# Kernel optimization log

Hardware: AMD Instinct MI355X
Metric: run time of the kernel (lower is better)

## Reference

```python
import jax, jax.numpy as jnp
import numpy as np

B, S, HID = 2, 2048, 2048
H, HKV, D = 16, 8, 128
RQ, RK, RV = 6, 2, 2
WINDOW = 1024
SOFTCAP = 50.0
SCALING = D ** -0.5
NEG_INF = -2.3819763e38  # gemma mask fill value (fp32 safe)


def _rope(x, cos, sin):
    # Gemma rotary: split last dim into two halves treated as (real, imag).
    d2 = x.shape[-1] // 2
    x1, x2 = x[..., :d2], x[..., d2:]
    return jnp.concatenate([x1 * cos - x2 * sin, x1 * sin + x2 * cos], axis=-1)


def setup_inputs() -> dict:
    key = jax.random.key(0)
    ks = jax.random.split(key, 8)
    hidden_states = jax.random.normal(ks[0], (B, S, HID), jnp.float32)
    w = 0.02
    W_A_q = jax.random.normal(ks[1], (HID, H * RQ), jnp.float32) * w
    W_B_q = jax.random.normal(ks[2], (HID, H * RQ * D), jnp.float32) * w
    W_A_k = jax.random.normal(ks[3], (HID, HKV * RK), jnp.float32) * w
    W_B_k = jax.random.normal(ks[4], (HID, RK * D), jnp.float32) * w
    W_A_v = jax.random.normal(ks[5], (HID, HKV * RV), jnp.float32) * w
    W_B_v = jax.random.normal(ks[6], (HID, RV * D), jnp.float32) * w
    W_o = jax.random.normal(ks[7], (H * D, HID), jnp.float32) * w
    # rotary tables (theta=10000)
    pos = jnp.arange(S, dtype=jnp.float32)
    inv = 1.0 / (10000.0 ** (jnp.arange(0, D, 2, dtype=jnp.float32) / D))
    ang = pos[:, None] * inv[None, :]  # [S, D/2]
    freqs_cos, freqs_sin = jnp.cos(ang), jnp.sin(ang)
    # causal + sliding-window additive mask [B,1,S,S]
    i = jnp.arange(S)[:, None]
    j = jnp.arange(S)[None, :]
    allowed = (j <= i) & (i - j < WINDOW)
    mask = jnp.where(allowed, 0.0, NEG_INF).astype(jnp.float32)
    mask = jnp.broadcast_to(mask[None, None], (B, 1, S, S))
    kv_write_indices = jnp.arange(S, dtype=jnp.int32)  # prefill: identity write
    return {
        'hidden_states': hidden_states, 'W_A_q': W_A_q, 'W_B_q': W_B_q,
        'W_A_k': W_A_k, 'W_B_k': W_B_k, 'W_A_v': W_A_v, 'W_B_v': W_B_v,
        'W_o': W_o, 'freqs_cos': freqs_cos, 'freqs_sin': freqs_sin,
        'mask': mask, 'kv_write_indices': kv_write_indices,
    }


def reference(hidden_states, W_A_q, W_B_q, W_A_k, W_B_k, W_A_v, W_B_v, W_o,
              freqs_cos, freqs_sin, mask, kv_write_indices):
    # Prefill: kv_write_indices == arange(S); factorized cache == current factors.
    b, s, _ = hidden_states.shape
    Aq = (hidden_states @ W_A_q).reshape(b, s, H, RQ)       # [b,s,H,Rq]
    Bq = (hidden_states @ W_B_q).reshape(b, s, H, RQ, D)    # [b,s,H,Rq,d]
    Ak = (hidden_states @ W_A_k).reshape(b, s, HKV, RK)
    Bk = (hidden_states @ W_B_k).reshape(b, s, RK, D)
    Av = (hidden_states @ W_A_v).reshape(b, s, HKV, RV)
    Bv = (hidden_states @ W_B_v).reshape(b, s, RV, D)
    # RoPE on the B factors (as in the original: applied to B_q rows and B_k rows)
    Bq = _rope(Bq, freqs_cos[:, None, None, :], freqs_sin[:, None, None, :])
    Bk = _rope(Bk, freqs_cos[:, None, :], freqs_sin[:, None, :])
    # Contract rank factors. Identical math to the per-head
    # einsum('bqrd,bksd->bqkrs') + einsum('bqr,bks,bqkrs->bqk') since the
    # bilinear form factorizes: sum_{r,s} Aq_r Ak_s <Bq_r, Bk_s> = <q, k>.
    q = jnp.einsum('bshr,bshrd->bshd', Aq, Bq)               # [b,s,H,d]
    k = jnp.einsum('bsgr,bsrd->bsgd', Ak, Bk)                # [b,s,Hkv,d]
    v = jnp.einsum('bsgr,bsrd->bsgd', Av, Bv)
    rep = H // HKV
    k = jnp.repeat(k, rep, axis=2)                            # GQA expand
    v = jnp.repeat(v, rep, axis=2)
    scores = jnp.einsum('bqhd,bkhd->bhqk', q, k) * SCALING
    scores = jnp.tanh(scores / SOFTCAP) * SOFTCAP             # logit softcap
    scores = scores + mask                                    # local sliding mask
    probs = jax.nn.softmax(scores, axis=-1)
    out = jnp.einsum('bhqk,bkhd->bqhd', probs, v).reshape(b, s, H * D)
    return out @ W_o
```

## Files before the change

kernel.cpp:

```cpp
#include <hip/hip_runtime.h>
#include <hip/hip_bf16.h>

#define S_LEN 2048
#define HID 2048
#define NB 2
#define NH 16
#define NKV 8
#define DH 128
#define RQ 6
#define KG 2048
#define SCALING 0.08838834764831845f

typedef __attribute__((ext_vector_type(8))) short s16x8;
typedef __attribute__((ext_vector_type(4))) float f32x4;

__device__ __forceinline__ float bf2f(ushort u) {
    union { unsigned int i; float f; } v; v.i = ((unsigned int)u) << 16; return v.f;
}
__device__ __forceinline__ ushort f2bf(float f) {
    __hip_bfloat16 h = __float2bfloat16(f);
    return *reinterpret_cast<ushort*>(&h);
}
__device__ __forceinline__ void g2lds16(const void* g, void* l) {
    __builtin_amdgcn_global_load_lds((const __attribute__((address_space(1))) void*)g,
                                     (__attribute__((address_space(3))) void*)l, 16, 0, 0);
}

__global__ void k_prep(const float* __restrict__ hs, const float* __restrict__ WAq,
                       const float* __restrict__ WAk, const float* __restrict__ WAv,
                       const float* __restrict__ WBk, const float* __restrict__ WBv,
                       const float* __restrict__ WBq, const float* __restrict__ Wo,
                       ushort* __restrict__ Xb, ushort* __restrict__ WtS,
                       ushort* __restrict__ WtBq, ushort* __restrict__ WtWo) {
    __shared__ ushort tile[64][68];
    int idx = blockIdx.x;
    int t = threadIdx.x;
    if (idx < 2048) {
#pragma unroll
        for (int j = 0; j < 4; ++j) {
            int i = idx * 1024 + t + j * 256;
            float4 v = ((const float4*)hs)[i];
            ushort4 o;
            o.x = f2bf(v.x); o.y = f2bf(v.y); o.z = f2bf(v.z); o.w = f2bf(v.w);
            ((ushort4*)Xb)[i] = o;
        }
        return;
    }
    idx -= 2048;
    const float* in; ushort* out; int Nin, rowOff;
    if (idx < 64)        { in = WAq; out = WtS;  Nin = 96;    rowOff = 0; }
    else if (idx < 96)   { idx -= 64;   in = WAk; out = WtS;  Nin = 16;    rowOff = 96; }
    else if (idx < 128)  { idx -= 96;   in = WAv; out = WtS;  Nin = 16;    rowOff = 112; }
    else if (idx < 256)  { idx -= 128;  in = WBk; out = WtS;  Nin = 256;   rowOff = 128; }
    else if (idx < 384)  { idx -= 256;  in = WBv; out = WtS;  Nin = 256;   rowOff = 384; }
    else if (idx < 6528) { idx -= 384;  in = WBq; out = WtBq; Nin = 12288; rowOff = 0; }
    else                 { idx -= 6528; in = Wo;  out = WtWo; Nin = 2048;  rowOff = 0; }
    int k0 = (idx & 31) * 64, n0 = (idx >> 5) * 64;
#pragma unroll
    for (int i = 0; i < 4; ++i) {
        int f = t + i * 256;
        int r = f >> 4;
        int c = (f & 15) * 4;
        int nn = n0 + c;
        float4 v = make_float4(0.f, 0.f, 0.f, 0.f);
        if (nn < Nin) v = *(const float4*)&in[(size_t)(k0 + r) * Nin + nn];
        ushort4 u;
        u.x = f2bf(v.x); u.y = f2bf(v.y); u.z = f2bf(v.z); u.w = f2bf(v.w);
        *(ushort4*)&tile[r][c] = u;
    }
    __syncthreads();
#pragma unroll
    for (int i = 0; i < 4; ++i) {
        int f = t + i * 256;
        int nr = f >> 4;
        int kc = (f & 15) * 4;
        int nn = n0 + nr;
        if (nn < Nin) {
            ushort4 u;
            u.x = tile[kc][nr]; u.y = tile[kc + 1][nr];
            u.z = tile[kc + 2][nr]; u.w = tile[kc + 3][nr];
            *(ushort4*)&out[(size_t)(rowOff + nn) * KG + k0 + kc] = u;
        }
    }
}

__device__ __forceinline__ void stc(float* p, float v) { *p = v; }
__device__ __forceinline__ void stc(ushort* p, float v) { *p = f2bf(v); }

template<typename OutT>
__global__ __launch_bounds__(256, 2) void k_gemm(const ushort* __restrict__ A,
                                                 const ushort* __restrict__ Bt,
                                                 OutT* __restrict__ C, int ldc) {
    __shared__ ushort lA[128 * 64];
    __shared__ ushort lB[128 * 64];
    const int tid = threadIdx.x;
    const int l = tid & 63, w = tid >> 6;
    const int gx = gridDim.x;
    int flat = blockIdx.y * gx + blockIdx.x;
    const int nwg = gx * gridDim.y;
    if ((nwg & 7) == 0) {
        int qq = nwg >> 3;
        flat = (flat & 7) * qq + (flat >> 3);
    }
    const int m0 = (flat % gx) * 128, n0 = (flat / gx) * 128;
    const int wm = w >> 1, wn = w & 1;
    f32x4 acc[4][4] = {};
    const int swz = 16 * ((tid & 7) ^ ((tid >> 3) & 7));
    const int rowbase = tid >> 3;

    for (int k0 = 0; k0 < KG; k0 += 64) {
#pragma unroll
        for (int i = 0; i < 4; ++i) {
            int row = rowbase + i * 32;
            const char* srcA = (const char*)A + (((size_t)(m0 + row) * KG + k0) * 2) + swz;
            g2lds16(srcA, (char*)lA + tid * 16 + i * 4096);
            const char* srcB = (const char*)Bt + (((size_t)(n0 + row) * KG + k0) * 2) + swz;
            g2lds16(srcB, (char*)lB + tid * 16 + i * 4096);
        }
        __syncthreads();
#pragma unroll
        for (int kk = 0; kk < 2; ++kk) {
            s16x8 af[4], bfr[4];
            const int kb = kk * 64 + (l >> 4) * 16;
#pragma unroll
            for (int mf = 0; mf < 4; ++mf) {
                int row = wm * 64 + mf * 16 + (l & 15);
                af[mf] = *(const s16x8*)((const char*)lA + row * 128 + (kb ^ ((row & 7) << 4)));
            }
#pragma unroll
            for (int nf = 0; nf < 4; ++nf) {
                int row = wn * 64 + nf * 16 + (l & 15);
                bfr[nf] = *(const s16x8*)((const char*)lB + row * 128 + (kb ^ ((row & 7) << 4)));
            }
#pragma unroll
            for (int mf = 0; mf < 4; ++mf)
#pragma unroll
                for (int nf = 0; nf < 4; ++nf)
                    acc[mf][nf] = __builtin_amdgcn_mfma_f32_16x16x32_bf16(af[mf], bfr[nf], acc[mf][nf], 0, 0, 0);
        }
        __syncthreads();
    }
#pragma unroll
    for (int mf = 0; mf < 4; ++mf)
#pragma unroll
        for (int r = 0; r < 4; ++r) {
            int row = m0 + wm * 64 + mf * 16 + (l >> 4) * 4 + r;
#pragma unroll
            for (int nf = 0; nf < 4; ++nf) {
                int col = n0 + wn * 64 + nf * 16 + (l & 15);
                stc(C + (size_t)row * ldc + col, acc[mf][nf][r]);
            }
        }
}

__global__ __launch_bounds__(512, 2) void k_gemm8(const ushort* __restrict__ A,
                                                  const ushort* __restrict__ Bt,
                                                  ushort* __restrict__ C, int ldc) {
    __shared__ char sB[131072];
    const int tid = threadIdx.x;
    const int l = tid & 63, wid = tid >> 6;
    const int wr = wid >> 2, wc = wid & 3;

    int flat = blockIdx.x;
    const int nwg = gridDim.x;
    if ((nwg & 7) == 0) {
        int qq = nwg >> 3;
        flat = (flat & 7) * qq + (flat >> 3);
    }
    const int m0 = (flat & 15) * 256;
    const int n0 = (flat >> 4) * 256;

    const int rb = tid >> 3;
    const int swz = 16 * ((tid & 7) ^ (rb & 7));
    const char* pAh[2][2];
    const char* pBh[2][2];
#pragma unroll
    for (int h = 0; h < 2; ++h)
#pragma unroll
        for (int j = 0; j < 2; ++j) {
            pAh[h][j] = (const char*)A + (size_t)(m0 + j * 128 + h * 64 + rb) * (KG * 2) + swz;
            pBh[h][j] = (const char*)Bt + (size_t)(n0 + (j * 2 + (tid >> 8)) * 64 + h * 32 + (rb & 31)) * (KG * 2) + swz;
        }

    f32x4 acc[8][4] = {};
    s16x8 af[4][2], bf[4][2];

    const int arow = (l & 15) * 128;
    const int kxor0 = (0 * 64 + (l >> 4) * 16) ^ ((l & 7) << 4);
    const int kxor1 = (1 * 64 + (l >> 4) * 16) ^ ((l & 7) << 4);

#define STG_A(T, D, H)                                                                     \
    do {                                                                                   \
        g2lds16(pAh[H][0] + (size_t)(T) * 128, sB + (D) * 65536 + (H) * 16384 + tid * 16); \
        g2lds16(pAh[H][1] + (size_t)(T) * 128, sB + (D) * 65536 + (H) * 16384 + 8192 + tid * 16); \
    } while (0)
#define STG_B(T, D, H)                                                                     \
    do {                                                                                   \
        g2lds16(pBh[H][0] + (size_t)(T) * 128, sB + (D) * 65536 + 32768 + (H) * 16384 + tid * 16); \
        g2lds16(pBh[H][1] + (size_t)(T) * 128, sB + (D) * 65536 + 32768 + (H) * 16384 + 8192 + tid * 16); \
    } while (0)
#define RD_A(D, MH)                                                                        \
    do {                                                                                   \
        const char* ab = sB + (D) * 65536 + (MH) * 16384 + wr * 8192;                      \
        _Pragma("unroll") for (int mi = 0; mi < 4; ++mi) {                                 \
            af[mi][0] = *(const s16x8*)(ab + mi * 2048 + arow + kxor0);                    \
            af[mi][1] = *(const s16x8*)(ab + mi * 2048 + arow + kxor1);                    \
        }                                                                                  \
    } while (0)
#define RD_B(D, BH)                                                                        \
    do {                                                                                   \
        const char* bb = sB + (D) * 65536 + 32768 + (BH) * 16384 + wc * 4096;              \
        _Pragma("unroll") for (int ni = 0; ni < 2; ++ni) {                                 \
            bf[(BH) * 2 + ni][0] = *(const s16x8*)(bb + ni * 2048 + arow + kxor0);         \
            bf[(BH) * 2 + ni][1] = *(const s16x8*)(bb + ni * 2048 + arow + kxor1);         \
        }                                                                                  \
    } while (0)
#define QMFMA(MQ, NQ)                                                                      \
    do {                                                                                   \
        __builtin_amdgcn_s_setprio(1);                                                     \
        _Pragma("unroll") for (int mi = 0; mi < 4; ++mi)                                   \
        _Pragma("unroll") for (int ni = 0; ni < 2; ++ni)                                   \
        _Pragma("unroll") for (int k2 = 0; k2 < 2; ++k2)                                   \
            acc[(MQ) * 4 + mi][(NQ) * 2 + ni] = __builtin_amdgcn_mfma_f32_16x16x32_bf16(   \
                af[mi][k2], bf[(NQ) * 2 + ni][k2], acc[(MQ) * 4 + mi][(NQ) * 2 + ni], 0, 0, 0); \
        __builtin_amdgcn_s_setprio(0);                                                     \
    } while (0)
#define BAR()                                   \
    do {                                        \
        asm volatile("" ::: "memory");          \
        __builtin_amdgcn_s_barrier();           \
        asm volatile("" ::: "memory");          \
    } while (0)
#define VM6() asm volatile("s_waitcnt vmcnt(6)" ::: "memory")
#define VM0() asm volatile("s_waitcnt vmcnt(0)" ::: "memory")

    STG_A(0, 0, 0); STG_A(0, 0, 1); STG_B(0, 0, 0); STG_B(0, 0, 1);
    STG_B(1, 1, 0); STG_B(1, 1, 1); STG_A(1, 1, 0);
    VM6();
    BAR();

    for (int i = 0; i < 16; ++i) {
        const bool last = (i == 15);
        const int t1 = 2 * i + 1, t2 = 2 * i + 2, t3 = 2 * i + 3;
        RD_A(0, 0); RD_B(0, 0);
        STG_A(t1, 1, 1);
        BAR(); QMFMA(0, 0); BAR();
        RD_B(0, 1);
        if (!last) STG_A(t2, 0, 0);
        BAR(); QMFMA(0, 1); BAR();
        RD_A(0, 1);
        if (!last) STG_B(t2, 0, 0);
        BAR(); QMFMA(1, 1); BAR();
        if (!last) { STG_B(t2, 0, 1); VM6(); } else { VM0(); }
        BAR(); QMFMA(1, 0); BAR();
        RD_A(1, 0); RD_B(1, 0);
        if (!last) STG_A(t2, 0, 1);
        BAR(); QMFMA(0, 0); BAR();
        RD_B(1, 1);
        if (!last) STG_B(t3, 1, 0);
        BAR(); QMFMA(0, 1); BAR();
        RD_A(1, 1);
        if (!last) STG_B(t3, 1, 1);
        BAR(); QMFMA(1, 1); BAR();
        if (!last) { STG_A(t3, 1, 0); VM6(); }
        BAR(); QMFMA(1, 0); BAR();
    }

#undef STG_A
#undef STG_B
#undef RD_A
#undef RD_B
#undef QMFMA

#pragma unroll
    for (int mf = 0; mf < 8; ++mf)
#pragma unroll
        for (int r = 0; r < 4; ++r) {
            int row = m0 + wr * 128 + mf * 16 + (l >> 4) * 4 + r;
#pragma unroll
            for (int nf = 0; nf < 4; ++nf) {
                int col = n0 + wc * 64 + nf * 16 + (l & 15);
                C[(size_t)row * ldc + col] = f2bf(acc[mf][nf][r]);
            }
        }
#undef BAR
#undef VM6
#undef VM0
}

__global__ __launch_bounds__(512, 2) void k_gemm8h(const ushort* __restrict__ A,
                                                   const ushort* __restrict__ Bt,
                                                   float* __restrict__ C, int ldc) {
    __shared__ char sB[98304];
    const int tid = threadIdx.x;
    const int l = tid & 63, wid = tid >> 6;
    const int wr = wid >> 2, wc = wid & 3;

    int flat = blockIdx.x;
    const int nwg = gridDim.x;
    if ((nwg & 7) == 0) {
        int qq = nwg >> 3;
        flat = (flat & 7) * qq + (flat >> 3);
    }
    const int m0 = (flat & 31) * 128;
    const int n0 = (flat >> 5) * 256;

    const int rb = tid >> 3;
    const int swz = 16 * ((tid & 7) ^ (rb & 7));
    const char* pA_[2];
    const char* pB_[2][2];
#pragma unroll
    for (int h = 0; h < 2; ++h) {
        pA_[h] = (const char*)A + (size_t)(m0 + (tid >> 8) * 64 + h * 32 + (rb & 31)) * (KG * 2) + swz;
#pragma unroll
        for (int j = 0; j < 2; ++j)
            pB_[h][j] = (const char*)Bt + (size_t)(n0 + (j * 2 + (tid >> 8)) * 64 + h * 32 + (rb & 31)) * (KG * 2) + swz;
    }

    f32x4 acc[4][4] = {};
    s16x8 af[2][2], bf[4][2];

    const int arow = (l & 15) * 128;
    const int kxor0 = ((l >> 4) * 16) ^ ((l & 7) << 4);
    const int kxor1 = (64 + (l >> 4) * 16) ^ ((l & 7) << 4);

#define STG_AH(T, D, H)                                                                    \
    g2lds16(pA_[H] + (size_t)(T) * 128, sB + (D) * 49152 + (H) * 8192 + tid * 16)
#define STG_BH(T, D, H)                                                                    \
    do {                                                                                   \
        g2lds16(pB_[H][0] + (size_t)(T) * 128, sB + (D) * 49152 + 16384 + (H) * 16384 + tid * 16); \
        g2lds16(pB_[H][1] + (size_t)(T) * 128, sB + (D) * 49152 + 16384 + (H) * 16384 + 8192 + tid * 16); \
    } while (0)
#define RD_AH(D, MH)                                                                       \
    do {                                                                                   \
        const char* ab = sB + (D) * 49152 + (MH) * 8192 + wr * 4096;                       \
        _Pragma("unroll") for (int mi = 0; mi < 2; ++mi) {                                 \
            af[mi][0] = *(const s16x8*)(ab + mi * 2048 + arow + kxor0);                    \
            af[mi][1] = *(const s16x8*)(ab + mi * 2048 + arow + kxor1);                    \
        }                                                                                  \
    } while (0)
#define RD_BH(D, BH)                                                                       \
    do {                                                                                   \
        const char* bb = sB + (D) * 49152 + 16384 + (BH) * 16384 + wc * 4096;              \
        _Pragma("unroll") for (int ni = 0; ni < 2; ++ni) {                                 \
            bf[(BH) * 2 + ni][0] = *(const s16x8*)(bb + ni * 2048 + arow + kxor0);         \
            bf[(BH) * 2 + ni][1] = *(const s16x8*)(bb + ni * 2048 + arow + kxor1);         \
        }                                                                                  \
    } while (0)
#define QMFMAH(MQ, NQ)                                                                     \
    do {                                                                                   \
        __builtin_amdgcn_s_setprio(1);                                                     \
        _Pragma("unroll") for (int mi = 0; mi < 2; ++mi)                                   \
        _Pragma("unroll") for (int ni = 0; ni < 2; ++ni)                                   \
        _Pragma("unroll") for (int k2 = 0; k2 < 2; ++k2)                                   \
            acc[(MQ) * 2 + mi][(NQ) * 2 + ni] = __builtin_amdgcn_mfma_f32_16x16x32_bf16(   \
                af[mi][k2], bf[(NQ) * 2 + ni][k2], acc[(MQ) * 2 + mi][(NQ) * 2 + ni], 0, 0, 0); \
        __builtin_amdgcn_s_setprio(0);                                                     \
    } while (0)
#define BAR()                                   \
    do {                                        \
        asm volatile("" ::: "memory");          \
        __builtin_amdgcn_s_barrier();           \
        asm volatile("" ::: "memory");          \
    } while (0)
#define VM5() asm volatile("s_waitcnt vmcnt(5)" ::: "memory")
#define VM0() asm volatile("s_waitcnt vmcnt(0)" ::: "memory")

    STG_AH(0, 0, 0); STG_AH(0, 0, 1); STG_BH(0, 0, 0); STG_BH(0, 0, 1);
    STG_BH(1, 1, 0); STG_BH(1, 1, 1); STG_AH(1, 1, 0);
    VM5();
    BAR();

    for (int i = 0; i < 16; ++i) {
        const bool last = (i == 15);
        const int t1 = 2 * i + 1, t2 = 2 * i + 2, t3 = 2 * i + 3;
        RD_AH(0, 0); RD_BH(0, 0);
        STG_AH(t1, 1, 1);
        BAR(); QMFMAH(0, 0); BAR();
        RD_BH(0, 1);
        if (!last) STG_AH(t2, 0, 0);
        BAR(); QMFMAH(0, 1); BAR();
        RD_AH(0, 1);
        if (!last) STG_BH(t2, 0, 0);
        BAR(); QMFMAH(1, 1); BAR();
        if (!last) { STG_BH(t2, 0, 1); VM5(); } else { VM0(); }
        BAR(); QMFMAH(1, 0); BAR();
        RD_AH(1, 0); RD_BH(1, 0);
        if (!last) STG_AH(t2, 0, 1);
        BAR(); QMFMAH(0, 0); BAR();
        RD_BH(1, 1);
        if (!last) STG_BH(t3, 1, 0);
        BAR(); QMFMAH(0, 1); BAR();
        RD_AH(1, 1);
        if (!last) STG_BH(t3, 1, 1);
        BAR(); QMFMAH(1, 1); BAR();
        if (!last) { STG_AH(t3, 1, 0); VM5(); }
        BAR(); QMFMAH(1, 0); BAR();
    }

#undef STG_AH
#undef STG_BH
#undef RD_AH
#undef RD_BH
#undef QMFMAH
#undef BAR
#undef VM5
#undef VM0

#pragma unroll
    for (int a = 0; a < 4; ++a)
#pragma unroll
        for (int r = 0; r < 4; ++r) {
            int row = m0 + wr * 64 + a * 16 + (l >> 4) * 4 + r;
#pragma unroll
            for (int b2 = 0; b2 < 4; ++b2) {
                int col = n0 + wc * 64 + b2 * 16 + (l & 15);
                C[(size_t)row * ldc + col] = acc[a][b2][r];
            }
        }
}

__global__ void k_contract_q(const ushort* __restrict__ bq, const float* __restrict__ small,
                             const float* __restrict__ cosT, const float* __restrict__ sinT,
                             ushort* __restrict__ q, int pitch, int hbase) {
    int srow = blockIdx.x;
    int b = srow >> 11, sl = srow & 2047;
    int t = threadIdx.x;
    int l = t & 63;
    int hloc = blockIdx.y * 4 + (t >> 6);
    int h = hbase + hloc;
    const ushort* bqr = bq + (size_t)srow * pitch + hloc * 768;
    const float* af = small + (size_t)srow * 640 + h * RQ;
    float y0 = 0.f, y1 = 0.f;
#pragma unroll
    for (int r = 0; r < RQ; ++r) {
        float a = af[r];
        ushort2 v = *(const ushort2*)&bqr[r * 128 + 2 * l];
        y0 += a * bf2f(v.x);
        y1 += a * bf2f(v.y);
    }
    float z0 = __shfl_xor(y0, 32);
    float z1 = __shfl_xor(y1, 32);
    int d = (l & 31) * 2;
    float2 cs = *(const float2*)&cosT[sl * 64 + d];
    float2 sn = *(const float2*)&sinT[sl * 64 + d];
    size_t o = ((size_t)(b * NH + h) * S_LEN + sl) * DH;
    ushort2 outv;
    if (l < 32) {
        outv.x = f2bf((y0 * cs.x - z0 * sn.x) * SCALING);
        outv.y = f2bf((y1 * cs.y - z1 * sn.y) * SCALING);
        *(ushort2*)&q[o + d] = outv;
    } else {
        outv.x = f2bf((z0 * sn.x + y0 * cs.x) * SCALING);
        outv.y = f2bf((z1 * sn.y + y1 * cs.y) * SCALING);
        *(ushort2*)&q[o + 64 + d] = outv;
    }
}

__global__ void k_contract_kv(const float* __restrict__ small, const float* __restrict__ cosT,
                              const float* __restrict__ sinT, ushort* __restrict__ kk,
                              ushort* __restrict__ vT) {
    int srow = blockIdx.x;
    int b = srow >> 11, sl = srow & 2047;
    int t = threadIdx.x;
    int d2 = t & 63, g = t >> 6;
    const float* row = small + (size_t)srow * 640;
    float k1 = 0.f, k2 = 0.f, v1 = 0.f, v2 = 0.f;
#pragma unroll
    for (int r = 0; r < 2; ++r) {
        float ak = row[96 + g * 2 + r];
        k1 += ak * row[128 + r * 128 + d2];
        k2 += ak * row[128 + r * 128 + 64 + d2];
        float av = row[112 + g * 2 + r];
        v1 += av * row[384 + r * 128 + d2];
        v2 += av * row[384 + r * 128 + 64 + d2];
    }
    float c = cosT[sl * 64 + d2], s = sinT[sl * 64 + d2];
    float kr1 = k1 * c - k2 * s, kr2 = k1 * s + k2 * c;
    size_t ko = ((size_t)(b * NKV + g) * S_LEN + sl) * DH + d2;
    kk[ko] = f2bf(kr1);
    kk[ko + 64] = f2bf(kr2);
    size_t vo = ((size_t)(b * NKV + g) * DH + d2) * S_LEN + sl;
    vT[vo] = f2bf(v1);
    vT[vo + (size_t)64 * S_LEN] = f2bf(v2);
}

__device__ __forceinline__ float softcap_p(float x) {
    float z = x * 0.02f;
    float z2 = z * z;
    float num = z * fmaf(z2, z2 + 105.f, 945.f);
    float den = fmaf(z2, fmaf(z2, 15.f, 420.f), 945.f);
    return __expf(fmaf(50.f, __fdividef(num, den), -50.f));
}

template<int FUSEQ>
__global__ __launch_bounds__(512, 2) void k_attn(const ushort* __restrict__ qsrc,
                                                 const float* __restrict__ small,
                                                 const float* __restrict__ cosT,
                                                 const float* __restrict__ sinT,
                                                 const ushort* __restrict__ kk,
                                                 const ushort* __restrict__ vT,
                                                 ushort* __restrict__ O) {
    __shared__ char sK[16384];
    __shared__ char sV[16384];
    __shared__ char sP[16384];
    const int f = blockIdx.x;
    const int xcd = f & 7;
    const int j = f >> 3;
    const int bg = xcd * 2 + (j >> 5);
    const int qb = 31 - (j & 31);
    const int b = bg >> 3, g = bg & 7;
    const int tid = threadIdx.x, l = tid & 63, w = tid >> 6;
    const int w4 = w & 3;
    const int h = g * 2 + (w >> 2);
    const int qs = qb * 64;
    const int q0 = qs + w4 * 16;

    s16x8 qf[4];
    if (FUSEQ) {
        const int row = q0 + (l & 15);
        const int srow = b * S_LEN + row;
        const float* af = small + (size_t)srow * 640 + h * RQ;
        const ushort* bqr = qsrc + (size_t)srow * 12288 + h * 768;
        const int k8 = (l >> 4) * 8;
#pragma unroll
        for (int grp = 0; grp < 2; ++grp) {
            const int dbase = grp * 32 + k8;
            float x1[8] = {}, x2[8] = {};
#pragma unroll
            for (int r = 0; r < RQ; ++r) {
                float a = af[r];
                s16x8 v1 = *(const s16x8*)&bqr[r * 128 + dbase];
                s16x8 v2 = *(const s16x8*)&bqr[r * 128 + 64 + dbase];
#pragma unroll
                for (int e = 0; e < 8; ++e) {
                    x1[e] = fmaf(a, bf2f((ushort)v1[e]), x1[e]);
                    x2[e] = fmaf(a, bf2f((ushort)v2[e]), x2[e]);
                }
            }
            const float* cp = &cosT[row * 64 + dbase];
            const float* sp = &sinT[row * 64 + dbase];
            s16x8 lo, hi;
#pragma unroll
            for (int e = 0; e < 8; ++e) {
                float c = cp[e], s = sp[e];
                lo[e] = (short)f2bf((x1[e] * c - x2[e] * s) * SCALING);
                hi[e] = (short)f2bf((x1[e] * s + x2[e] * c) * SCALING);
            }
            qf[grp] = lo;
            qf[grp + 2] = hi;
        }
    } else {
        const ushort* qbase = qsrc + ((size_t)(b * NH + h) * S_LEN) * DH;
        const char* qrow = (const char*)(qbase + (size_t)(q0 + (l & 15)) * DH);
#pragma unroll
        for (int ds = 0; ds < 4; ++ds)
            qf[ds] = *(const s16x8*)(qrow + ds * 64 + (l >> 4) * 16);
    }

    f32x4 acc[8] = {};
    float lrow[4] = {0.f, 0.f, 0.f, 0.f};

    const size_t kgbase = ((size_t)(b * NKV + g) * S_LEN) * DH * 2;
    const size_t vgbase = ((size_t)(b * NKV + g) * DH) * S_LEN * 2;

    const int jt0 = (qs > 1023) ? ((qs - 1023) >> 6) : 0;
    const int ibase = q0 + (l >> 4) * 4;

    for (int jt = jt0; jt <= qb; ++jt) {
#pragma unroll
        for (int i = 0; i < 2; ++i) {
            int row = (tid >> 4) + i * 32;
            int colb = (tid & 15) * 16;
            const char* src = (const char*)kk + kgbase + ((size_t)(jt * 64 + row)) * 256 + (colb ^ ((row & 7) << 4));
            g2lds16(src, sK + tid * 16 + i * 8192);
        }
#pragma unroll
        for (int i = 0; i < 2; ++i) {
            int row = (tid >> 3) + i * 64;
            int colb = (tid & 7) * 16;
            const char* src = (const char*)vT + vgbase + (size_t)row * 4096 + (size_t)jt * 128 + (colb ^ ((row & 7) << 4));
            g2lds16(src, sV + tid * 16 + i * 8192);
        }
        __syncthreads();

        const bool diag = (jt == qb);
        const bool wclip = (jt == jt0) && (qs > 1023);

        f32x4 sc[4] = {};
#pragma unroll
        for (int ct = 0; ct < 4; ++ct) {
            if (diag && ct > w4) continue;
            f32x4 z = {};
            int row = ct * 16 + (l & 15);
#pragma unroll
            for (int ds = 0; ds < 4; ++ds) {
                int kb = ds * 64 + (l >> 4) * 16;
                s16x8 kf = *(const s16x8*)(sK + row * 256 + (kb ^ ((row & 7) << 4)));
                z = __builtin_amdgcn_mfma_f32_16x16x32_bf16(qf[ds], kf, z, 0, 0, 0);
            }
            sc[ct] = z;
        }
        float p[4][4];
        if (!diag && !wclip) {
#pragma unroll
            for (int ct = 0; ct < 4; ++ct)
#pragma unroll
                for (int r = 0; r < 4; ++r) {
                    float pe = softcap_p(sc[ct][r]);
                    p[ct][r] = pe;
                    lrow[r] += pe;
                }
        } else if (diag) {
#pragma unroll
            for (int ct = 0; ct < 4; ++ct) {
                if (ct > w4) {
#pragma unroll
                    for (int r = 0; r < 4; ++r) p[ct][r] = 0.f;
                    continue;
                }
                int j2 = jt * 64 + ct * 16 + (l & 15);
#pragma unroll
                for (int r = 0; r < 4; ++r) {
                    float pe = softcap_p(sc[ct][r]);
                    pe = (j2 <= ibase + r) ? pe : 0.f;
                    p[ct][r] = pe;
                    lrow[r] += pe;
                }
            }
        } else {
#pragma unroll
            for (int ct = 0; ct < 4; ++ct) {
                int j2 = jt * 64 + ct * 16 + (l & 15);
#pragma unroll
                for (int r = 0; r < 4; ++r) {
                    float pe = softcap_p(sc[ct][r]);
                    pe = (j2 > ibase + r - 1024) ? pe : 0.f;
                    p[ct][r] = pe;
                    lrow[r] += pe;
                }
            }
        }
#pragma unroll
        for (int ct = 0; ct < 4; ++ct) {
            int col = ct * 16 + (l & 15);
#pragma unroll
            for (int r = 0; r < 4; ++r) {
                int row = (l >> 4) * 4 + r;
                *(ushort*)(sP + w * 2048 + row * 128 + ((col * 2) ^ ((row & 7) << 4))) = f2bf(p[ct][r]);
            }
        }
#pragma unroll
        for (int s2 = 0; s2 < 2; ++s2) {
            int rowp = l & 15;
            int kb = s2 * 64 + (l >> 4) * 16;
            s16x8 pf = *(const s16x8*)(sP + w * 2048 + rowp * 128 + (kb ^ ((rowp & 7) << 4)));
#pragma unroll
            for (int dt = 0; dt < 8; ++dt) {
                int d = dt * 16 + (l & 15);
                s16x8 vf = *(const s16x8*)(sV + d * 128 + (kb ^ ((d & 7) << 4)));
                acc[dt] = __builtin_amdgcn_mfma_f32_16x16x32_bf16(pf, vf, acc[dt], 0, 0, 0);
            }
        }
        __syncthreads();
    }
#pragma unroll
    for (int r = 0; r < 4; ++r) {
        float rs = lrow[r];
        rs += __shfl_xor(rs, 1); rs += __shfl_xor(rs, 2);
        rs += __shfl_xor(rs, 4); rs += __shfl_xor(rs, 8);
        lrow[r] = rs;
    }
#pragma unroll
    for (int r = 0; r < 4; ++r) {
        int row = qs + w4 * 16 + (l >> 4) * 4 + r;
        float inv = 1.f / lrow[r];
#pragma unroll
        for (int dt = 0; dt < 8; ++dt)
            O[((size_t)(b * S_LEN + row)) * HID + h * DH + dt * 16 + (l & 15)] = f2bf(acc[dt][r] * inv);
    }
}

extern "C" void kernel_launch(void* const* d_in, const int* in_sizes, int n_in,
                              void* d_out, int out_size, void* d_ws, size_t ws_size,
                              hipStream_t stream) {
    (void)in_sizes; (void)n_in; (void)out_size;
    const float* hs  = (const float*)d_in[0];
    const float* WAq = (const float*)d_in[1];
    const float* WBq = (const float*)d_in[2];
    const float* WAk = (const float*)d_in[3];
    const float* WBk = (const float*)d_in[4];
    const float* WAv = (const float*)d_in[5];
    const float* WBv = (const float*)d_in[6];
    const float* Wo  = (const float*)d_in[7];
    const float* fc  = (const float*)d_in[8];
    const float* fs  = (const float*)d_in[9];

    char* ws = (char*)d_ws;
    ushort* Xb    = (ushort*)(ws + 0);
    ushort* WtS   = (ushort*)(ws + 16777216);
    ushort* WtBq  = (ushort*)(ws + 19398656);
    ushort* WtWo  = (ushort*)(ws + 69730304);
    float*  Small = (float*) (ws + 78118912);
    ushort* BqC   = (ushort*)(ws + 88604672);

    const bool bigws = (ws_size >= 239599616ull);
    size_t tail = bigws ? 189267968ull : 113770496ull;
    ushort* qB  = (ushort*)(ws + tail);
    ushort* kB  = (ushort*)(ws + tail + 16777216);
    ushort* vTB = (ushort*)(ws + tail + 25165824);
    ushort* OB  = (ushort*)(ws + tail + 33554432);

    k_prep<<<9600, 256, 0, stream>>>(hs, WAq, WAk, WAv, WBk, WBv, WBq, Wo,
                                     Xb, WtS, WtBq, WtWo);

    k_gemm<float><<<dim3(32, 5), 256, 0, stream>>>(Xb, WtS, Small, 640);
    k_contract_kv<<<4096, 512, 0, stream>>>(Small, fc, fs, kB, vTB);

    if (bigws) {
        k_gemm8<<<768, 512, 0, stream>>>(Xb, WtBq, BqC, 12288);
        k_attn<1><<<512, 512, 0, stream>>>(BqC, Small, fc, fs, kB, vTB, OB);
    } else {
        for (int c = 0; c < 4; ++c) {
            k_gemm8<<<192, 512, 0, stream>>>(Xb, WtBq + (size_t)c * 3072 * KG, BqC, 3072);
            k_contract_q<<<dim3(4096, 1), 256, 0, stream>>>(BqC, Small, fc, fs, qB, 3072, c * 4);
        }
        k_attn<0><<<512, 512, 0, stream>>>(qB, Small, fc, fs, kB, vTB, OB);
    }

    k_gemm8h<<<256, 512, 0, stream>>>(OB, WtWo, (float*)d_out, 2048);
}
```

Measured before the change: 431.9 us.

## Double-buffer K/V tiles in attention kernel to overlap loads with MFMA

```diff
diff --git a/kernel.cpp b/kernel.cpp
--- a/kernel.cpp
+++ b/kernel.cpp
@@ -501,8 +501,8 @@
                                                  const ushort* __restrict__ kk,
                                                  const ushort* __restrict__ vT,
                                                  ushort* __restrict__ O) {
-    __shared__ char sK[16384];
-    __shared__ char sV[16384];
+    __shared__ char sK[2][16384];
+    __shared__ char sV[2][16384];
     __shared__ char sP[16384];
     const int f = blockIdx.x;
     const int xcd = f & 7;
@@ -567,22 +567,35 @@
     const int jt0 = (qs > 1023) ? ((qs - 1023) >> 6) : 0;
     const int ibase = q0 + (l >> 4) * 4;
 
+    const int krow0 = tid >> 4, kcolb = (tid & 15) * 16;
+    const int vrow0 = tid >> 3, vcolb = (tid & 7) * 16;
+
+#define STAGE_KV(JT, SLOT)                                                                   \
+    do {                                                                                     \
+        _Pragma("unroll")                                                                    \
+        for (int i = 0; i < 2; ++i) {                                                        \
+            int row = krow0 + i * 32;                                                        \
+            const char* src = (const char*)kk + kgbase + ((size_t)((JT) * 64 + row)) * 256   \
+                              + (kcolb ^ ((row & 7) << 4));                                  \
+            g2lds16(src, &sK[SLOT][tid * 16 + i * 8192]);                                    \
+        }                                                                                    \
+        _Pragma("unroll")                                                                    \
+        for (int i = 0; i < 2; ++i) {                                                        \
+            int row = vrow0 + i * 64;                                                        \
+            const char* src = (const char*)vT + vgbase + (size_t)row * 4096                  \
+                              + (size_t)(JT) * 128 + (vcolb ^ ((row & 7) << 4));             \
+            g2lds16(src, &sV[SLOT][tid * 16 + i * 8192]);                                    \
+        }                                                                                    \
+    } while (0)
+
+    STAGE_KV(jt0, 0);
+    asm volatile("s_waitcnt vmcnt(0)" ::: "memory");
+    __builtin_amdgcn_s_barrier();
+    asm volatile("" ::: "memory");
+
     for (int jt = jt0; jt <= qb; ++jt) {
-#pragma unroll
-        for (int i = 0; i < 2; ++i) {
-            int row = (tid >> 4) + i * 32;
-            int colb = (tid & 15) * 16;
-            const char* src = (const char*)kk + kgbase + ((size_t)(jt * 64 + row)) * 256 + (colb ^ ((row & 7) << 4));
-            g2lds16(src, sK + tid * 16 + i * 8192);
-        }
-#pragma unroll
-        for (int i = 0; i < 2; ++i) {
-            int row = (tid >> 3) + i * 64;
-            int colb = (tid & 7) * 16;
-            const char* src = (const char*)vT + vgbase + (size_t)row * 4096 + (size_t)jt * 128 + (colb ^ ((row & 7) << 4));
-            g2lds16(src, sV + tid * 16 + i * 8192);
-        }
-        __syncthreads();
+        const int cur = (jt - jt0) & 1;
+        if (jt < qb) STAGE_KV(jt + 1, cur ^ 1);
 
         const bool diag = (jt == qb);
         const bool wclip = (jt == jt0) && (qs > 1023);
@@ -596,7 +609,7 @@
 #pragma unroll
             for (int ds = 0; ds < 4; ++ds) {
                 int kb = ds * 64 + (l >> 4) * 16;
-                s16x8 kf = *(const s16x8*)(sK + row * 256 + (kb ^ ((row & 7) << 4)));
+                s16x8 kf = *(const s16x8*)(&sK[cur][row * 256 + (kb ^ ((row & 7) << 4))]);
                 z = __builtin_amdgcn_mfma_f32_16x16x32_bf16(qf[ds], kf, z, 0, 0, 0);
             }
             sc[ct] = z;
@@ -658,12 +671,17 @@
 #pragma unroll
             for (int dt = 0; dt < 8; ++dt) {
                 int d = dt * 16 + (l & 15);
-                s16x8 vf = *(const s16x8*)(sV + d * 128 + (kb ^ ((d & 7) << 4)));
+                s16x8 vf = *(const s16x8*)(&sV[cur][d * 128 + (kb ^ ((d & 7) << 4))]);
                 acc[dt] = __builtin_amdgcn_mfma_f32_16x16x32_bf16(pf, vf, acc[dt], 0, 0, 0);
             }
         }
-        __syncthreads();
-    }
+
+        asm volatile("s_waitcnt vmcnt(0)" ::: "memory");
+        __builtin_amdgcn_s_barrier();
+        asm volatile("" ::: "memory");
+    }
+#undef STAGE_KV
+
 #pragma unroll
     for (int r = 0; r < 4; ++r) {
         float rs = lrow[r];
```

After: 421.3 us. 2.5% less time.
